# Optimization experiments

Measured on AMD Instinct MI355X. Metric: run time of the kernel, lower is better.

Reference implementation:

```python
import jax, jax.numpy as jnp
import numpy as np

HID = 2048      # hidden_size
H = 16          # num_heads == num_kv_heads (stack in fwd forces MHA)
DH = HID // H   # head_size = 128
QKV = 3 * H * DH  # 6144
THETA = 10000.0
EPS = 1e-5      # flash-attn RMSNorm default eps
B, L = 4, 2048


def setup_inputs() -> dict:
    key = jax.random.key(0)
    k1, k2, k3 = jax.random.split(key, 3)
    hidden_states = jax.random.normal(k1, (B, L, HID), dtype=jnp.float32)
    # weights stored as (in, out); scaled like a typical init so activations stay sane
    W_qkvg = jax.random.normal(k2, (HID, QKV + HID), dtype=jnp.float32) * 0.02
    W_out = jax.random.normal(k3, (HID, HID), dtype=jnp.float32) * 0.02
    return {"hidden_states": hidden_states, "W_qkvg": W_qkvg, "W_out": W_out}


def _rmsnorm(x):
    # elementwise_affine=False: pure rms normalization over head dim
    return x * jax.lax.rsqrt(jnp.mean(x * x, axis=-1, keepdims=True) + EPS)


def _rope(x, seqlen_offset=0):
    # x: (B, L, H, DH), non-interleaved (GPT-NeoX style rotate-half)
    half = DH // 2
    inv_freq = 1.0 / (THETA ** (jnp.arange(half, dtype=jnp.float32) * 2.0 / DH))
    pos = jnp.arange(seqlen_offset, seqlen_offset + x.shape[1], dtype=jnp.float32)
    ang = pos[:, None] * inv_freq[None, :]                  # (L, half)
    cos = jnp.cos(ang)[None, :, None, :]                    # (1,L,1,half)
    sin = jnp.sin(ang)[None, :, None, :]
    x1, x2 = x[..., :half], x[..., half:]
    return jnp.concatenate([x1 * cos - x2 * sin, x1 * sin + x2 * cos], axis=-1)


def _attention_forward(hidden_states, W_qkvg, W_out):
    b, l, _ = hidden_states.shape
    proj = hidden_states @ W_qkvg                           # (B,L,QKV+HID)
    qkv_flat, gate = proj[..., :QKV], proj[..., QKV:]
    gate = jax.nn.sigmoid(gate)
    qkv = qkv_flat.reshape(b, l, 3 * H, DH)
    q, k, v = qkv[:, :, :H], qkv[:, :, H:2 * H], qkv[:, :, 2 * H:]
    q = _rope(_rmsnorm(q))
    k = _rope(_rmsnorm(k))
    # causal softmax attention (math of flash_attn_func)
    scores = jnp.einsum('blhd,bmhd->bhlm', q, k) / np.sqrt(DH).astype(np.float32)
    causal = jnp.tril(jnp.ones((l, l), dtype=bool))
    scores = jnp.where(causal[None, None], scores, jnp.finfo(scores.dtype).min)
    attn = jax.nn.softmax(scores, axis=-1)
    out = jnp.einsum('bhlm,bmhd->blhd', attn, v).reshape(b, l, HID)
    out = out * gate
    return out @ W_out


def reference(hidden_states, W_qkvg, W_out):
    return _attention_forward(hidden_states, W_qkvg, W_out)
```

## Files before the change

### kernel.cpp

```cpp
#include <hip/hip_runtime.h>


typedef __attribute__((ext_vector_type(8))) short bf16x8;
typedef __attribute__((ext_vector_type(4))) float f32x4;
typedef __attribute__((ext_vector_type(4))) unsigned short us4;

#if __has_builtin(__builtin_amdgcn_exp2f)
#define EXP2(x) __builtin_amdgcn_exp2f(x)
#else
#define EXP2(x) exp2f(x)
#endif

__device__ __forceinline__ unsigned short f2bf(float f) {
    unsigned int x = __float_as_uint(f);
    unsigned int r = x + 0x7fffu + ((x >> 16) & 1u);
    return (unsigned short)(r >> 16);
}
__device__ __forceinline__ unsigned short f2bf_fast(float f) {
    return (unsigned short)((__float_as_uint(f) + 0x8000u) >> 16);
}
__device__ __forceinline__ float bf2f(unsigned short u) {
    return __uint_as_float(((unsigned int)u) << 16);
}

__device__ __forceinline__ void gll16(const unsigned short* g, unsigned short* l) {
    __builtin_amdgcn_global_load_lds(
        (const __attribute__((address_space(1))) unsigned int*)g,
        (__attribute__((address_space(3))) unsigned int*)l, 16, 0, 0);
}

__device__ __forceinline__ void barx() {
    asm volatile("" ::: "memory");
    __builtin_amdgcn_s_barrier();
    asm volatile("" ::: "memory");
}
#define LGKM0() asm volatile("s_waitcnt lgkmcnt(0)" ::: "memory")
#define VM6()   asm volatile("s_waitcnt vmcnt(6)" ::: "memory")
#define VM4()   asm volatile("s_waitcnt vmcnt(4)" ::: "memory")
#define VM0()   asm volatile("s_waitcnt vmcnt(0)" ::: "memory")

__global__ __launch_bounds__(256) void cvt_bf16(const float* __restrict__ in,
                                                unsigned short* __restrict__ out) {
    int i = blockIdx.x * 256 + threadIdx.x;
    float4 v = ((const float4*)in)[i];
    us4 r;
    r[0] = f2bf(v.x); r[1] = f2bf(v.y); r[2] = f2bf(v.z); r[3] = f2bf(v.w);
    ((us4*)out)[i] = r;
}

__global__ __launch_bounds__(256) void transpose_cvt(const float* __restrict__ in,
                                                     unsigned short* __restrict__ out,
                                                     int R, int C) {
    __shared__ float t[32][33];
    int c0 = blockIdx.x * 32, r0 = blockIdx.y * 32;
    int tx = threadIdx.x, ty = threadIdx.y;
#pragma unroll
    for (int i = 0; i < 4; i++)
        t[ty + i * 8][tx] = in[(size_t)(r0 + ty + i * 8) * C + c0 + tx];
    __syncthreads();
#pragma unroll
    for (int i = 0; i < 4; i++)
        out[(size_t)(c0 + ty + i * 8) * R + r0 + tx] = f2bf(t[tx][ty + i * 8]);
}

__device__ __forceinline__ void gemm256_core(const unsigned short* __restrict__ A,
                                             const unsigned short* __restrict__ Bt,
                                             int K, int rowA0, int colB0,
                                             unsigned short* sm,
                                             f32x4 acc[8][4]) {
    const int tid = threadIdx.x;
    const int w = tid >> 6, lane = tid & 63;
    const int quad = lane >> 4, l15 = lane & 15;
    const int wm = w >> 2, wn = w & 3;
    const int lr = lane >> 3;
    const int lc = ((lane & 7) ^ lr) * 8;
    const int NT = K >> 6;

    const unsigned short* pA = A  + (size_t)(rowA0 + w * 16 + lr) * K + lc;
    const unsigned short* pB = Bt + (size_t)(colB0 + w * 16 + lr) * K + lc;
    unsigned short* lw = sm + w * 16 * 64;

#define STAGE(tt, isB, h)                                                       \
    do {                                                                        \
        const unsigned short* gp_ = ((isB) ? pB : pA) +                         \
            (size_t)(h) * 128 * K + (size_t)(tt) * 64;                          \
        unsigned short* lp_ = lw + (((tt) & 1) * 4 + (isB) * 2 + (h)) * 8192;   \
        gll16(gp_, lp_);                                                        \
        gll16(gp_ + (size_t)8 * K, lp_ + 8 * 64);                               \
    } while (0)

    STAGE(0, 1, 0); STAGE(0, 1, 1); STAGE(0, 0, 0); STAGE(0, 0, 1);
    STAGE(1, 1, 0); STAGE(1, 1, 1); STAGE(1, 0, 0);
    VM6();
    barx();

    for (int t = 0; t < NT; ++t) {
        const unsigned short* Asl = sm + ((t & 1) * 4 + wm) * 8192;
        const unsigned short* Bsl = sm + ((t & 1) * 4 + 2 + (wn >> 1)) * 8192;
        bf16x8 bfrag[4][2];
#pragma unroll
        for (int q = 0; q < 4; ++q) {
            if (q == 0) {
#pragma unroll
                for (int nj = 0; nj < 4; ++nj)
#pragma unroll
                    for (int kk = 0; kk < 2; ++kk) {
                        int r = (wn & 1) * 64 + nj * 16 + l15;
                        bfrag[nj][kk] = *(const bf16x8*)&Bsl[r * 64 +
                            (((kk * 4 + quad) ^ (r & 7)) * 8)];
                    }
            }
            bf16x8 afr[2][2];
#pragma unroll
            for (int mi = 0; mi < 2; ++mi)
#pragma unroll
                for (int kk = 0; kk < 2; ++kk) {
                    int r = q * 32 + mi * 16 + l15;
                    afr[mi][kk] = *(const bf16x8*)&Asl[r * 64 +
                        (((kk * 4 + quad) ^ (r & 7)) * 8)];
                }
            if (q == 0)      { if (t + 1 < NT) STAGE(t + 1, 0, 1); }
            else if (q == 1) { if (t + 2 < NT) STAGE(t + 2, 1, 0); }
            else if (q == 2) { if (t + 2 < NT) STAGE(t + 2, 1, 1); }
            else {
                if (t + 2 < NT)      { STAGE(t + 2, 0, 0); VM6(); }
                else if (t + 1 < NT) { VM0(); }
            }
            barx();
            LGKM0();
            __builtin_amdgcn_s_setprio(1);
#pragma unroll
            for (int mi = 0; mi < 2; ++mi)
#pragma unroll
                for (int nj = 0; nj < 4; ++nj)
#pragma unroll
                    for (int kk = 0; kk < 2; ++kk)
                        acc[q * 2 + mi][nj] = __builtin_amdgcn_mfma_f32_16x16x32_bf16(
                            afr[mi][kk], bfrag[nj][kk], acc[q * 2 + mi][nj], 0, 0, 0);
            __builtin_amdgcn_s_setprio(0);
            barx();
        }
    }
#undef STAGE
}

__global__ __launch_bounds__(512) void gemm_qkvg(const unsigned short* __restrict__ A,
                                                 const unsigned short* __restrict__ Bt,
                                                 unsigned short* __restrict__ Qb,
                                                 unsigned short* __restrict__ Kb,
                                                 unsigned short* __restrict__ Vt,
                                                 unsigned short* __restrict__ Gb) {
    __shared__ unsigned short sm[8 * 8192];
    f32x4 acc[8][4];
    f32x4 z = {0.f, 0.f, 0.f, 0.f};
#pragma unroll
    for (int i = 0; i < 8; i++)
#pragma unroll
        for (int j = 0; j < 4; j++) acc[i][j] = z;

    const int g = blockIdx.y * 32 + blockIdx.x;
    const int xcd = g & 7, lo = g >> 3;
    const int bx = xcd * 4 + (lo & 3), by = lo >> 2;
    const int rowA0 = by * 256, colB0 = bx * 256;
    gemm256_core(A, Bt, 2048, rowA0, colB0, sm, acc);

    const int tid = threadIdx.x, w = tid >> 6, lane = tid & 63;
    const int quad = lane >> 4, l15 = lane & 15;
    const int wm = w >> 2, wn = w & 3;
    const int sec = colB0 >> 11;
    const int hbase = (colB0 & 2047) >> 7;

    if (sec == 2) {
#pragma unroll
        for (int mi = 0; mi < 8; ++mi)
#pragma unroll
            for (int nj = 0; nj < 4; ++nj)
#pragma unroll
                for (int i = 0; i < 4; ++i) {
                    int ll = wm * 128 + mi * 16 + quad * 4 + i;
                    int c  = wn * 64 + nj * 16 + l15;
                    int hh = c >> 7, d = c & 127;
                    sm[hh * 32768 + d * 256 + (((ll >> 3) ^ (d & 31)) * 8) + (ll & 7)] =
                        f2bf(acc[mi][nj][i]);
                }
        __syncthreads();
        const int b_ = rowA0 >> 11, l0 = rowA0 & 2047;
        const int d = tid >> 2, part = tid & 3;
#pragma unroll
        for (int hh = 0; hh < 2; ++hh) {
            unsigned short* drow = Vt +
                ((size_t)(b_ * 16 + hbase + hh) * 128 + d) * 2048 + l0 + part * 64;
#pragma unroll
            for (int j = 0; j < 8; ++j) {
                int chunk = part * 8 + j;
                *(bf16x8*)(drow + j * 8) =
                    *(const bf16x8*)&sm[hh * 32768 + d * 256 + ((chunk ^ (d & 31)) * 8)];
            }
        }
    } else if (sec == 3) {
#pragma unroll
        for (int mi = 0; mi < 8; ++mi)
#pragma unroll
            for (int nj = 0; nj < 4; ++nj)
#pragma unroll
                for (int i = 0; i < 4; ++i) {
                    int rowg = rowA0 + wm * 128 + mi * 16 + quad * 4 + i;
                    int c = wn * 64 + nj * 16 + l15;
                    int h = hbase + (c >> 7), d = c & 127;
                    float gv = 1.f / (1.f + __expf(-acc[mi][nj][i]));
                    Gb[((size_t)rowg << 11) + h * 128 + d] = f2bf(gv);
                }
    } else {
        unsigned short* dst = (sec == 0) ? Qb : Kb;
#pragma unroll
        for (int mi = 0; mi < 8; ++mi)
#pragma unroll
            for (int nj = 0; nj < 4; ++nj)
#pragma unroll
                for (int i = 0; i < 4; ++i) {
                    int rowg = rowA0 + wm * 128 + mi * 16 + quad * 4 + i;
                    int c = wn * 64 + nj * 16 + l15;
                    int h = hbase + (c >> 7), d = c & 127;
                    int b_ = rowg >> 11, l_ = rowg & 2047;
                    dst[(((size_t)(b_ * 16 + h) * 2048 + l_) << 7) + d] =
                        f2bf(acc[mi][nj][i]);
                }
    }
}

__global__ __launch_bounds__(512) void gemm_out(const unsigned short* __restrict__ A,
                                                const unsigned short* __restrict__ Bt,
                                                float* __restrict__ C) {
    __shared__ unsigned short sm[8 * 8192];
    f32x4 acc[8][4];
    f32x4 z = {0.f, 0.f, 0.f, 0.f};
#pragma unroll
    for (int i = 0; i < 8; i++)
#pragma unroll
        for (int j = 0; j < 4; j++) acc[i][j] = z;

    const int g = blockIdx.y * 8 + blockIdx.x;
    const int gs = (g & 7) * 32 + (g >> 3);
    const int bx = gs & 7, by = gs >> 3;
    const int rowA0 = by * 256, colB0 = bx * 256;
    gemm256_core(A, Bt, 2048, rowA0, colB0, sm, acc);

    const int tid = threadIdx.x, w = tid >> 6, lane = tid & 63;
    const int quad = lane >> 4, l15 = lane & 15;
    const int wm = w >> 2, wn = w & 3;
#pragma unroll
    for (int mi = 0; mi < 8; ++mi)
#pragma unroll
        for (int nj = 0; nj < 4; ++nj)
#pragma unroll
            for (int i = 0; i < 4; ++i) {
                int rowg = rowA0 + wm * 128 + mi * 16 + quad * 4 + i;
                int col = colB0 + wn * 64 + nj * 16 + l15;
                C[(size_t)rowg * 2048 + col] = acc[mi][nj][i];
            }
}

__global__ __launch_bounds__(256) void rmsnorm_rope(unsigned short* __restrict__ Qp,
                                                    unsigned short* __restrict__ Kp) {
    unsigned short* X = blockIdx.y ? Kp : Qp;
    const int tid = threadIdx.x;
    const int row = blockIdx.x * 4 + (tid >> 6);
    const int lane = tid & 63;
    unsigned short* p = X + (size_t)row * 128;
    const int l_ = row & 2047;
    float x1 = bf2f(p[lane]);
    float x2 = bf2f(p[lane + 64]);
    float ss = x1 * x1 + x2 * x2;
#pragma unroll
    for (int off = 32; off >= 1; off >>= 1) ss += __shfl_xor(ss, off, 64);
    float r = rsqrtf(ss * (1.f / 128.f) + 1e-5f);
    x1 *= r; x2 *= r;
    float inv = exp2f(-(float)lane * (13.287712379549449f / 64.f));
    float ang = (float)l_ * inv;
    float sn, cs;
    sincosf(ang, &sn, &cs);
    p[lane]      = f2bf(x1 * cs - x2 * sn);
    p[lane + 64] = f2bf(x1 * sn + x2 * cs);
}

__global__ __launch_bounds__(512) void fa_kernel(const unsigned short* __restrict__ Q,
                                                 const unsigned short* __restrict__ K,
                                                 const unsigned short* __restrict__ Vt,
                                                 const unsigned short* __restrict__ G,
                                                 unsigned short* __restrict__ Og) {
    __shared__ unsigned short Ks[2][64 * 128];
    __shared__ unsigned short Vs[2][128 * 64];
    __shared__ unsigned short Ps[256 * 32];
    const int g = blockIdx.x;
    const int bh = (g & 7) | ((g >> 6) << 3);
    const int qc = (g >> 3) & 7;
    const int tid = threadIdx.x, w = tid >> 6, lane = tid & 63;
    const int quad = lane >> 4, l15 = lane & 15;
    const int sw = l15 & 7;
    const int qrow0 = qc * 256 + w * 32;
    const float CS = 0.12751740395609812f;

    bf16x8 qf[2][4];
#pragma unroll
    for (int mi = 0; mi < 2; mi++)
#pragma unroll
        for (int kt = 0; kt < 4; kt++)
            qf[mi][kt] = *(const bf16x8*)(Q + ((size_t)bh * 2048 + qrow0 + mi * 16 + l15) * 128
                                             + kt * 32 + quad * 8);

    f32x4 o[2][8];
    f32x4 z = {0.f, 0.f, 0.f, 0.f};
#pragma unroll
    for (int mi = 0; mi < 2; mi++)
#pragma unroll
        for (int nj = 0; nj < 8; nj++) o[mi][nj] = z;
    float rowsum[2][4];
#pragma unroll
    for (int mi = 0; mi < 2; mi++)
#pragma unroll
        for (int i = 0; i < 4; i++) rowsum[mi][i] = 0.f;

    const unsigned short* Kbase = K + (size_t)bh * 2048 * 128;
    const unsigned short* Vtb   = Vt + (size_t)bh * 128 * 2048;

    const int krow = lane >> 4, kc = lane & 15;
    const int vrow = lane >> 3, vc = lane & 7;

#define STAGE_KV(jj, buf)                                                        \
    do {                                                                         \
        _Pragma("unroll")                                                        \
        for (int i_ = 0; i_ < 2; i_++) {                                         \
            int r0_ = w * 8 + i_ * 4;                                            \
            int row_ = r0_ + krow;                                               \
            int cs_ = (kc & 8) | ((kc & 7) ^ (row_ & 7));                        \
            gll16(Kbase + (size_t)((jj) * 64 + row_) * 128 + cs_ * 8,            \
                  &Ks[buf][r0_ * 128]);                                          \
        }                                                                        \
        _Pragma("unroll")                                                        \
        for (int i_ = 0; i_ < 2; i_++) {                                         \
            int r0_ = w * 16 + i_ * 8;                                           \
            int row_ = r0_ + vrow;                                               \
            gll16(Vtb + (size_t)row_ * 2048 + (jj) * 64 + ((vc ^ (row_ & 7)) * 8), \
                  &Vs[buf][r0_ * 64]);                                           \
        }                                                                        \
    } while (0)

    const int pr0 = w * 32 + l15, pr1 = pr0 + 16;
    const int pk0 = (pr0 >> 1) & 3, pk1 = (pr1 >> 1) & 3;

    const int NJ = 4 * (qc + 1);

    STAGE_KV(0, 0);

    for (int j = 0; j < NJ; j++) {
        const int cur = j & 1;
        if (j + 1 < NJ) { STAGE_KV(j + 1, cur ^ 1); VM4(); }
        else            { VM0(); }
        barx();

        if (j * 64 < qrow0 + 32) {
            f32x4 s[2][4];
#pragma unroll
            for (int mi = 0; mi < 2; mi++)
#pragma unroll
                for (int nj = 0; nj < 4; nj++) s[mi][nj] = z;
#pragma unroll
            for (int kt = 0; kt < 4; kt++)
#pragma unroll
                for (int nj = 0; nj < 4; nj++) {
                    bf16x8 bfr = *(const bf16x8*)&Ks[cur][(nj * 16 + l15) * 128 +
                                                         (((kt * 4 + quad) ^ sw) * 8)];
                    s[0][nj] = __builtin_amdgcn_mfma_f32_16x16x32_bf16(qf[0][kt], bfr, s[0][nj], 0, 0, 0);
                    s[1][nj] = __builtin_amdgcn_mfma_f32_16x16x32_bf16(qf[1][kt], bfr, s[1][nj], 0, 0, 0);
                }

            const bool diag = (j * 64 + 63 > qrow0);
#pragma unroll
            for (int hh = 0; hh < 2; hh++) {
#pragma unroll
                for (int mi = 0; mi < 2; mi++)
#pragma unroll
                    for (int njh = 0; njh < 2; njh++) {
                        const int nj = hh * 2 + njh;
#pragma unroll
                        for (int i = 0; i < 4; i++) {
                            float pp = EXP2(s[mi][nj][i] * CS);
                            int row_l = mi * 16 + quad * 4 + i;
                            if (diag) {
                                int col_g = j * 64 + nj * 16 + l15;
                                if (col_g > qrow0 + row_l) pp = 0.f;
                            }
                            rowsum[mi][i] += pp;
                            int row = w * 32 + row_l;
                            int kv = njh * 16 + l15;
                            Ps[row * 32 + ((((kv >> 3) ^ ((row >> 1) & 3)) * 8)) + (kv & 7)] =
                                f2bf_fast(pp);
                        }
                    }
                bf16x8 a0 = *(const bf16x8*)&Ps[pr0 * 32 + ((quad ^ pk0) * 8)];
                bf16x8 a1 = *(const bf16x8*)&Ps[pr1 * 32 + ((quad ^ pk1) * 8)];
#pragma unroll
                for (int nj = 0; nj < 8; nj++) {
                    bf16x8 bfr = *(const bf16x8*)&Vs[cur][(nj * 16 + l15) * 64 +
                                                          (((hh * 4 + quad) ^ sw) * 8)];
                    o[0][nj] = __builtin_amdgcn_mfma_f32_16x16x32_bf16(a0, bfr, o[0][nj], 0, 0, 0);
                    o[1][nj] = __builtin_amdgcn_mfma_f32_16x16x32_bf16(a1, bfr, o[1][nj], 0, 0, 0);
                }
            }
        }
        barx();
    }
#undef STAGE_KV

    const int b_ = bh >> 4, h = bh & 15;
#pragma unroll
    for (int mi = 0; mi < 2; mi++)
#pragma unroll
        for (int i = 0; i < 4; i++) {
            float t = rowsum[mi][i];
#pragma unroll
            for (int off = 1; off < 16; off <<= 1) t += __shfl_xor(t, off, 16);
            float rl = 1.f / t;
            int l_ = qrow0 + mi * 16 + quad * 4 + i;
#pragma unroll
            for (int nj = 0; nj < 8; nj++) {
                int d = nj * 16 + l15;
                size_t gi = ((size_t)(b_ * 2048 + l_) * 2048) + h * 128 + d;
                Og[gi] = f2bf(o[mi][nj][i] * rl * bf2f(G[gi]));
            }
        }
}

extern "C" void kernel_launch(void* const* d_in, const int* in_sizes, int n_in,
                              void* d_out, int out_size, void* d_ws, size_t ws_size,
                              hipStream_t stream) {
    const float* X  = (const float*)d_in[0];
    const float* Wq = (const float*)d_in[1];
    const float* Wo = (const float*)d_in[2];
    float* out = (float*)d_out;

    char* ws = (char*)d_ws;
    const size_t SZ = 33554432ull;
    unsigned short* Xb  = (unsigned short*)(ws);
    unsigned short* Wqt = (unsigned short*)(ws + SZ);
    unsigned short* Wot = (unsigned short*)(ws + 2 * SZ);
    unsigned short* Qb  = (unsigned short*)(ws + 2 * SZ + 8388608ull);
    unsigned short* Kb  = (unsigned short*)(ws + 3 * SZ + 8388608ull);
    unsigned short* Vt  = (unsigned short*)(ws + 4 * SZ + 8388608ull);
    unsigned short* Gb  = (unsigned short*)(ws + 5 * SZ + 8388608ull);
    unsigned short* OG  = Xb;

    cvt_bf16<<<16384, 256, 0, stream>>>(X, Xb);
    transpose_cvt<<<dim3(256, 64), dim3(32, 8), 0, stream>>>(Wq, Wqt, 2048, 8192);
    transpose_cvt<<<dim3(64, 64),  dim3(32, 8), 0, stream>>>(Wo, Wot, 2048, 2048);

    gemm_qkvg<<<dim3(32, 32), 512, 0, stream>>>(Xb, Wqt, Qb, Kb, Vt, Gb);

    rmsnorm_rope<<<dim3(32768, 2), 256, 0, stream>>>(Qb, Kb);

    fa_kernel<<<512, 512, 0, stream>>>(Qb, Kb, Vt, Gb, OG);

    gemm_out<<<dim3(8, 32), 512, 0, stream>>>(OG, Wot, out);
}
```

Measured before the change: 715.6 us.

## Vectorize rmsnorm_rope, remap QKVG GEMM tiles per XCD, add MFMA setprio

The rmsnorm_rope kernel now has 16 lanes handle each row. Each lane loads and stores 8 bf16 values as one 128-bit access, so the kernel needs a quarter as many blocks. The rotate-half partner is fetched with a lane shuffle. The QKVG GEMM swaps its XCD-aware block remap for one that gives each XCD a contiguous range of 128 tiles, which changes L2 locality. The flash-attention kernel raises wave priority around its MFMA sections to encourage overlap with the softmax work of other waves.

```diff
diff --git a/kernel.cpp b/kernel.cpp
--- a/kernel.cpp
+++ b/kernel.cpp
@@ -159,8 +159,8 @@
         for (int j = 0; j < 4; j++) acc[i][j] = z;
 
     const int g = blockIdx.y * 32 + blockIdx.x;
-    const int xcd = g & 7, lo = g >> 3;
-    const int bx = xcd * 4 + (lo & 3), by = lo >> 2;
+    const int gs = (g & 7) * 128 + (g >> 3);
+    const int bx = gs & 31, by = gs >> 5;
     const int rowA0 = by * 256, colB0 = bx * 256;
     gemm256_core(A, Bt, 2048, rowA0, colB0, sm, acc);
 
@@ -264,23 +264,44 @@
                                                     unsigned short* __restrict__ Kp) {
     unsigned short* X = blockIdx.y ? Kp : Qp;
     const int tid = threadIdx.x;
-    const int row = blockIdx.x * 4 + (tid >> 6);
-    const int lane = tid & 63;
-    unsigned short* p = X + (size_t)row * 128;
-    const int l_ = row & 2047;
-    float x1 = bf2f(p[lane]);
-    float x2 = bf2f(p[lane + 64]);
-    float ss = x1 * x1 + x2 * x2;
-#pragma unroll
-    for (int off = 32; off >= 1; off >>= 1) ss += __shfl_xor(ss, off, 64);
-    float r = rsqrtf(ss * (1.f / 128.f) + 1e-5f);
-    x1 *= r; x2 *= r;
-    float inv = exp2f(-(float)lane * (13.287712379549449f / 64.f));
-    float ang = (float)l_ * inv;
-    float sn, cs;
-    sincosf(ang, &sn, &cs);
-    p[lane]      = f2bf(x1 * cs - x2 * sn);
-    p[lane + 64] = f2bf(x1 * sn + x2 * cs);
+    const int wv = tid >> 6, lane = tid & 63;
+    const int rgrp = lane >> 4;
+    const int l16 = lane & 15;
+    const int sub = l16 >> 3, l8 = l16 & 7;
+    const int row = blockIdx.x * 16 + wv * 4 + rgrp;
+    unsigned short* p = X + (size_t)row * 128 + sub * 64 + l8 * 8;
+    const int pos = row & 2047;
+
+    bf16x8 v = *(const bf16x8*)p;
+    float x[8];
+    float ss = 0.f;
+#pragma unroll
+    for (int j = 0; j < 8; j++) {
+        x[j] = bf2f((unsigned short)v[j]);
+        ss += x[j] * x[j];
+    }
+#pragma unroll
+    for (int off = 8; off >= 1; off >>= 1) ss += __shfl_xor(ss, off, 16);
+    const float r = rsqrtf(ss * (1.f / 128.f) + 1e-5f);
+
+    float xs[8], xp[8];
+#pragma unroll
+    for (int j = 0; j < 8; j++) xs[j] = x[j] * r;
+#pragma unroll
+    for (int j = 0; j < 8; j++) xp[j] = __shfl_xor(xs[j], 8, 16);
+
+    const float sgn = sub ? 1.f : -1.f;
+    bf16x8 o;
+#pragma unroll
+    for (int j = 0; j < 8; j++) {
+        int k = l8 * 8 + j;
+        float inv = exp2f(-(float)k * (13.287712379549449f / 64.f));
+        float ang = (float)pos * inv;
+        float sn, cs;
+        sincosf(ang, &sn, &cs);
+        o[j] = (short)f2bf(xs[j] * cs + xp[j] * (sgn * sn));
+    }
+    *(bf16x8*)p = o;
 }
 
 __global__ __launch_bounds__(512) void fa_kernel(const unsigned short* __restrict__ Q,
@@ -364,6 +385,7 @@
             for (int mi = 0; mi < 2; mi++)
 #pragma unroll
                 for (int nj = 0; nj < 4; nj++) s[mi][nj] = z;
+            __builtin_amdgcn_s_setprio(1);
 #pragma unroll
             for (int kt = 0; kt < 4; kt++)
 #pragma unroll
@@ -373,6 +395,7 @@
                     s[0][nj] = __builtin_amdgcn_mfma_f32_16x16x32_bf16(qf[0][kt], bfr, s[0][nj], 0, 0, 0);
                     s[1][nj] = __builtin_amdgcn_mfma_f32_16x16x32_bf16(qf[1][kt], bfr, s[1][nj], 0, 0, 0);
                 }
+            __builtin_amdgcn_s_setprio(0);
 
             const bool diag = (j * 64 + 63 > qrow0);
 #pragma unroll
@@ -399,6 +422,7 @@
                     }
                 bf16x8 a0 = *(const bf16x8*)&Ps[pr0 * 32 + ((quad ^ pk0) * 8)];
                 bf16x8 a1 = *(const bf16x8*)&Ps[pr1 * 32 + ((quad ^ pk1) * 8)];
+                __builtin_amdgcn_s_setprio(1);
 #pragma unroll
                 for (int nj = 0; nj < 8; nj++) {
                     bf16x8 bfr = *(const bf16x8*)&Vs[cur][(nj * 16 + l15) * 64 +
@@ -406,6 +430,7 @@
                     o[0][nj] = __builtin_amdgcn_mfma_f32_16x16x32_bf16(a0, bfr, o[0][nj], 0, 0, 0);
                     o[1][nj] = __builtin_amdgcn_mfma_f32_16x16x32_bf16(a1, bfr, o[1][nj], 0, 0, 0);
                 }
+                __builtin_amdgcn_s_setprio(0);
             }
         }
         barx();
@@ -456,7 +481,7 @@
 
     gemm_qkvg<<<dim3(32, 32), 512, 0, stream>>>(Xb, Wqt, Qb, Kb, Vt, Gb);
 
-    rmsnorm_rope<<<dim3(32768, 2), 256, 0, stream>>>(Qb, Kb);
+    rmsnorm_rope<<<dim3(8192, 2), 256, 0, stream>>>(Qb, Kb);
 
     fa_kernel<<<512, 512, 0, stream>>>(Qb, Kb, Vt, Gb, OG);
 
```

Result: faster. 692.7 us (-3.2%).
